# Optimization experiments

Measured on AMD Instinct MI355X. Metric: run time of the kernel, lower is better.

The kernel has to match this reference:

```python
import jax, jax.numpy as jnp
import numpy as np

N_OSC = 32
CONV = 1000.0  # convergence_factor


def _cpg_ode(y, ia, ifr, cw, pb):
    # Faithful to CPGOde.forward, including its unpacking order:
    # (amplitudes, amplitudes_dot, phases) = (y[:n], y[n:2n], y[2n:3n])
    n = N_OSC
    a = y[:n]
    a_dot = y[n:2 * n]
    ph = y[2 * n:3 * n]
    phase_dots = ifr + jnp.sum(a[:, None] * cw * jnp.sin(ph[None, :] - ph[:, None] - pb), axis=1)
    a_dd = CONV * (CONV / 4.0 * (ia - a) - a_dot)
    # states_to_tensor(amplitudes_dot, phase_dots, amplitudes_dot_dot)
    return jnp.concatenate([a_dot, phase_dots, a_dd])


def _rk4_38_step(f, y, h):
    # torchdiffeq 'rk4' = rk4_alt_step_func (3/8 rule), one step over t=[0, h]
    k1 = f(y)
    k2 = f(y + h * k1 / 3.0)
    k3 = f(y + h * (k2 - k1 / 3.0))
    k4 = f(y + h * (k1 - k2 + k3))
    return y + h * 0.125 * (k1 + 3.0 * (k2 + k3) + k4)


def _mlp(x, Ws, bs):
    # Linear stack with ReLU between layers, none after the last
    for i, (W, b) in enumerate(zip(Ws, bs)):
        x = W @ x + b
        if i < len(Ws) - 1:
            x = jax.nn.relu(x)
    return x


def _init_linear(key, fan_in, fan_out):
    kW, kb = jax.random.split(key)
    bound = 1.0 / np.sqrt(fan_in)
    W = jax.random.uniform(kW, (fan_out, fan_in), minval=-bound, maxval=bound, dtype=jnp.float32)
    b = jax.random.uniform(kb, (fan_out,), minval=-bound, maxval=bound, dtype=jnp.float32)
    return W, b


def setup_inputs() -> dict:
    key = jax.random.key(0)
    ks = jax.random.split(key, 10)
    n = N_OSC
    n_params = 2 * n + 2 * n * n  # 2112
    in_dims = [2049, 4096, 4096, n_params]  # input_layers[0]+1, ..., final param layer
    out_dims = [2 * n, 2048, 2048, 1024]
    inp = {}
    inp["state"] = jax.random.normal(ks[0], (3 * n,), dtype=jnp.float32) * 0.1
    inp["x"] = jax.random.normal(ks[1], (2048,), dtype=jnp.float32)
    inp["timestep"] = jnp.array(0.01, dtype=jnp.float32)
    for i in range(3):
        W, b = _init_linear(ks[2 + i], in_dims[i], in_dims[i + 1])
        inp[f"in_W{i}"] = W
        inp[f"in_b{i}"] = b
    for i in range(3):
        W, b = _init_linear(ks[5 + i], out_dims[i], out_dims[i + 1])
        inp[f"out_W{i}"] = W
        inp[f"out_b{i}"] = b
    return inp


def reference(state, x, timestep,
              in_W0, in_b0, in_W1, in_b1, in_W2, in_b2,
              out_W0, out_b0, out_W1, out_b1, out_W2, out_b2):
    n = N_OSC
    # append timestep scalar to the input features
    x = jnp.concatenate([x, timestep[None]])
    params = _mlp(x, [in_W0, in_W1, in_W2], [in_b0, in_b1, in_b2])
    ia = params[:n]
    ifr = params[n:2 * n]
    cw = params[2 * n:2 * n + n * n].reshape(n, n)
    pb = params[2 * n + n * n:].reshape(n, n)
    f = lambda y: _cpg_ode(y, ia, ifr, cw, pb)
    new_state = _rk4_38_step(f, state, timestep)
    a = new_state[:n]
    ph = new_state[n:2 * n]
    cpg_out = jnp.concatenate([a * jnp.cos(ph), a * jnp.sin(ph)])
    out = _mlp(cpg_out, [out_W0, out_W1, out_W2], [out_b0, out_b1, out_b2])
    return (jax.lax.stop_gradient(new_state), out)
```

## Files before the change

### kernel.cpp

```cpp
#include <hip/hip_runtime.h>
#include <hip/hip_bf16.h>
#include <stdint.h>

typedef unsigned short ushort_t;

__device__ __forceinline__ float bf2f(ushort_t u) {
    union { unsigned int i; float f; } v;
    v.i = ((unsigned int)u) << 16;
    return v.f;
}

__device__ __forceinline__ ushort_t f2bf(float f) {
    __hip_bfloat16 h = __float2bfloat16(f);
    return *reinterpret_cast<ushort_t*>(&h);
}

__device__ __forceinline__ float read_ts_robust(const void* ts) {
    float bf = bf2f(((const ushort_t*)ts)[0]);
    float ab = fabsf(bf);
    if (isfinite(bf) && ab > 1e-6f && ab < 1e3f) return bf;
    return ((const float*)ts)[0];
}

__global__ void detect_kernel(const ushort_t* __restrict__ W, int* __restrict__ flag) {
    if (threadIdx.x == 0 && blockIdx.x == 0) {
        int cnt = 0;
        for (int k = 0; k < 64; k++) {
            float v = bf2f(W[2 * k]);
            if (!(fabsf(v) < 1.0f)) cnt++;
        }
        *flag = (cnt >= 8) ? 1 : 0;
    }
}

__global__ void prep_x_kernel(const ushort_t* __restrict__ xb,
                              const void* __restrict__ ts,
                              float* __restrict__ xf, int n,
                              const int* __restrict__ flag) {
    int f = *flag;
    int i = blockIdx.x * blockDim.x + threadIdx.x;
    if (i < n) xf[i] = f ? ((const float*)xb)[i] : bf2f(xb[i]);
    if (i == 0) xf[n] = f ? ((const float*)ts)[0] : read_ts_robust(ts);
}

__global__ __launch_bounds__(256) void gemv_kernel(
    const ushort_t* __restrict__ W, const ushort_t* __restrict__ B,
    const float* __restrict__ x, float* __restrict__ y,
    void* __restrict__ outbuf, int out_off, int rows, int cols, int relu,
    const int* __restrict__ flag)
{
    int f = *flag;
    int wave = threadIdx.x >> 6;
    int lane = threadIdx.x & 63;
    int row = blockIdx.x * 4 + wave;
    if (row >= rows) return;

    float sum = 0.0f;

    if (f) {
        const float* w = (const float*)W + (size_t)row * (size_t)cols;
        int mis = (int)(((uintptr_t)w & 15) >> 2);
        int start = (4 - mis) & 3;
        if (start > cols) start = cols;
        if (lane < start) sum += w[lane] * x[lane];
        int nv = (cols - start) >> 2;
        const float4* wv = (const float4*)(w + start);
        for (int g = lane; g < nv; g += 64) {
            float4 u = wv[g];
            const float* xp = x + start + g * 4;
            sum += u.x * xp[0] + u.y * xp[1] + u.z * xp[2] + u.w * xp[3];
        }
        int t = start + nv * 4 + lane;
        if (t < cols) sum += w[t] * x[t];
    } else {
        const ushort_t* w = W + (size_t)row * (size_t)cols;
        int mis = (int)(((uintptr_t)w & 15) >> 1);
        int start = (8 - mis) & 7;
        if (start > cols) start = cols;
        if (lane < start) sum += bf2f(w[lane]) * x[lane];
        int nv = (cols - start) >> 3;
        const uint4* wv = (const uint4*)(w + start);
        for (int g = lane; g < nv; g += 64) {
            uint4 u = wv[g];
            const float* xp = x + start + g * 8;
            sum += bf2f((ushort_t)(u.x & 0xffff)) * xp[0];
            sum += bf2f((ushort_t)(u.x >> 16))    * xp[1];
            sum += bf2f((ushort_t)(u.y & 0xffff)) * xp[2];
            sum += bf2f((ushort_t)(u.y >> 16))    * xp[3];
            sum += bf2f((ushort_t)(u.z & 0xffff)) * xp[4];
            sum += bf2f((ushort_t)(u.z >> 16))    * xp[5];
            sum += bf2f((ushort_t)(u.w & 0xffff)) * xp[6];
            sum += bf2f((ushort_t)(u.w >> 16))    * xp[7];
        }
        int t = start + nv * 8 + lane;
        if (t < cols) sum += bf2f(w[t]) * x[t];
    }

    #pragma unroll
    for (int off = 32; off > 0; off >>= 1)
        sum += __shfl_down(sum, off);

    if (lane == 0) {
        float r = sum + (f ? ((const float*)B)[row] : bf2f(B[row]));
        if (relu) r = fmaxf(r, 0.0f);
        if (y) y[row] = r;
        if (outbuf) {
            if (f) ((float*)outbuf)[out_off + row] = r;
            else   ((ushort_t*)outbuf)[out_off + row] = f2bf(r);
        }
    }
}

__global__ __launch_bounds__(64) void ode_kernel(
    const ushort_t* __restrict__ state, const void* __restrict__ ts,
    const float* __restrict__ params, float* __restrict__ cpg,
    void* __restrict__ out_state, const int* __restrict__ flag)
{
    const float CONV = 1000.0f;
    __shared__ float s_y[96];
    int f = *flag;
    int t = threadIdx.x;
    bool act = (t < 32);
    int i = t;
    float h = f ? ((const float*)ts)[0] : read_ts_robust(ts);

    float ia = 0.f, ifr = 0.f;
    float cwr[32], pbr[32];
    float y0a = 0.f, y0b = 0.f, y0c = 0.f;

    if (act) {
        ia = params[i];
        ifr = params[32 + i];
        #pragma unroll
        for (int j = 0; j < 32; j++) {
            cwr[j] = params[64 + i * 32 + j];
            pbr[j] = params[1088 + i * 32 + j];
        }
        const float* sf = (const float*)state;
        y0a = f ? sf[i]      : bf2f(state[i]);
        y0b = f ? sf[32 + i] : bf2f(state[32 + i]);
        y0c = f ? sf[64 + i] : bf2f(state[64 + i]);
        s_y[i] = y0a; s_y[32 + i] = y0b; s_y[64 + i] = y0c;
    }
    __syncthreads();

    float k1a=0,k1b=0,k1c=0, k2a=0,k2b=0,k2c=0, k3a=0,k3b=0,k3c=0, k4a=0,k4b=0,k4c=0;

    auto evalf = [&](float& fa, float& fb, float& fc) {
        float a  = s_y[i];
        float ad = s_y[32 + i];
        float ph = s_y[64 + i];
        float ssum = 0.0f;
        #pragma unroll
        for (int j = 0; j < 32; j++) {
            ssum += cwr[j] * sinf(s_y[64 + j] - ph - pbr[j]);
        }
        fa = ad;
        fb = ifr + a * ssum;
        fc = CONV * (CONV * 0.25f * (ia - a) - ad);
    };

    if (act) evalf(k1a, k1b, k1c);
    __syncthreads();
    if (act) {
        s_y[i]      = y0a + h * k1a / 3.0f;
        s_y[32 + i] = y0b + h * k1b / 3.0f;
        s_y[64 + i] = y0c + h * k1c / 3.0f;
    }
    __syncthreads();
    if (act) evalf(k2a, k2b, k2c);
    __syncthreads();
    if (act) {
        s_y[i]      = y0a + h * (k2a - k1a / 3.0f);
        s_y[32 + i] = y0b + h * (k2b - k1b / 3.0f);
        s_y[64 + i] = y0c + h * (k2c - k1c / 3.0f);
    }
    __syncthreads();
    if (act) evalf(k3a, k3b, k3c);
    __syncthreads();
    if (act) {
        s_y[i]      = y0a + h * (k1a - k2a + k3a);
        s_y[32 + i] = y0b + h * (k1b - k2b + k3b);
        s_y[64 + i] = y0c + h * (k1c - k2c + k3c);
    }
    __syncthreads();
    if (act) evalf(k4a, k4b, k4c);

    if (act) {
        float na = y0a + h * 0.125f * (k1a + 3.0f * (k2a + k3a) + k4a);
        float nb = y0b + h * 0.125f * (k1b + 3.0f * (k2b + k3b) + k4b);
        float nc = y0c + h * 0.125f * (k1c + 3.0f * (k2c + k3c) + k4c);
        if (f) {
            float* fo = (float*)out_state;
            fo[i] = na; fo[32 + i] = nb; fo[64 + i] = nc;
        } else {
            ushort_t* bo = (ushort_t*)out_state;
            bo[i] = f2bf(na); bo[32 + i] = f2bf(nb); bo[64 + i] = f2bf(nc);
        }
        cpg[i]      = na * cosf(nb);
        cpg[32 + i] = na * sinf(nb);
    }
}

extern "C" void kernel_launch(void* const* d_in, const int* in_sizes, int n_in,
                              void* d_out, int out_size, void* d_ws, size_t ws_size,
                              hipStream_t stream) {
    const ushort_t* state = (const ushort_t*)d_in[0];
    const ushort_t* x     = (const ushort_t*)d_in[1];
    const void*     ts    = d_in[2];
    const ushort_t* inW0  = (const ushort_t*)d_in[3];
    const ushort_t* inb0  = (const ushort_t*)d_in[4];
    const ushort_t* inW1  = (const ushort_t*)d_in[5];
    const ushort_t* inb1  = (const ushort_t*)d_in[6];
    const ushort_t* inW2  = (const ushort_t*)d_in[7];
    const ushort_t* inb2  = (const ushort_t*)d_in[8];
    const ushort_t* oW0   = (const ushort_t*)d_in[9];
    const ushort_t* ob0   = (const ushort_t*)d_in[10];
    const ushort_t* oW1   = (const ushort_t*)d_in[11];
    const ushort_t* ob1   = (const ushort_t*)d_in[12];
    const ushort_t* oW2   = (const ushort_t*)d_in[13];
    const ushort_t* ob2   = (const ushort_t*)d_in[14];

    float* ws  = (float*)d_ws;
    float* xf  = ws;
    float* h0  = ws + 2064;
    float* h1  = ws + 6160;
    float* pr  = ws + 10256;
    float* cpg = ws + 12368;
    float* g0  = ws + 12432;
    float* g1  = ws + 14480;
    int*   flg = (int*)(ws + 16536);

    detect_kernel<<<1, 64, 0, stream>>>(inW1, flg);
    prep_x_kernel<<<9, 256, 0, stream>>>(x, ts, xf, 2048, flg);
    gemv_kernel<<<1024, 256, 0, stream>>>(inW0, inb0, xf, h0, nullptr, 0, 4096, 2049, 1, flg);
    gemv_kernel<<<1024, 256, 0, stream>>>(inW1, inb1, h0, h1, nullptr, 0, 4096, 4096, 1, flg);
    gemv_kernel<<<528,  256, 0, stream>>>(inW2, inb2, h1, pr, nullptr, 0, 2112, 4096, 0, flg);
    ode_kernel<<<1, 64, 0, stream>>>(state, ts, pr, cpg, d_out, flg);
    gemv_kernel<<<512,  256, 0, stream>>>(oW0, ob0, cpg, g0, nullptr, 0, 2048, 64, 1, flg);
    gemv_kernel<<<512,  256, 0, stream>>>(oW1, ob1, g0, g1, nullptr, 0, 2048, 2048, 1, flg);
    gemv_kernel<<<256,  256, 0, stream>>>(oW2, ob2, g1, nullptr, d_out, 96, 1024, 2048, 0, flg);
}
```

Baseline: 263.4 us.

## Drop bf16 detection path, use block-per-row fp32 GEMV and sincos-factored ODE

Removes the runtime dtype detection kernel, the x-prep kernel and the bf16 branches, and assumes fp32 inputs throughout. The timestep column is folded directly into the first GEMV. Each GEMV now uses a full 256-thread block per row with 4-way unrolled float4 loads and a shared-memory cross-wave reduction, instead of one wave per row. The ODE kernel precomputes sin/cos of the phase biases and uses angle-difference identities, so it needs only one sincos per oscillator per stage instead of 32 sinf calls. This trades launch count and dtype flexibility for more memory parallelism per row. It breaks if the inputs are actually bf16.

```diff
diff --git a/kernel.cpp b/kernel.cpp
--- a/kernel.cpp
+++ b/kernel.cpp
@@ -1,202 +1,146 @@
 #include <hip/hip_runtime.h>
-#include <hip/hip_bf16.h>
 #include <stdint.h>
 
-typedef unsigned short ushort_t;
+template<int RELU, int TS>
+__global__ __launch_bounds__(256) void gemv_k(
+    const float* __restrict__ W, const float* __restrict__ B,
+    const float* __restrict__ x, const float* __restrict__ ts,
+    float* __restrict__ y, int cols)
+{
+    int tid = threadIdx.x;
+    int row = blockIdx.x;
+    int n = TS ? cols - 1 : cols;
+    const float* w = W + (size_t)row * (size_t)cols;
 
-__device__ __forceinline__ float bf2f(ushort_t u) {
-    union { unsigned int i; float f; } v;
-    v.i = ((unsigned int)u) << 16;
-    return v.f;
-}
+    int mis = (int)(((uintptr_t)w >> 2) & 3);
+    int start = (4 - mis) & 3;
+    if (start > n) start = n;
 
-__device__ __forceinline__ ushort_t f2bf(float f) {
-    __hip_bfloat16 h = __float2bfloat16(f);
-    return *reinterpret_cast<ushort_t*>(&h);
-}
+    float sum = 0.0f;
+    if (tid < start) sum += w[tid] * x[tid];
 
-__device__ __forceinline__ float read_ts_robust(const void* ts) {
-    float bf = bf2f(((const ushort_t*)ts)[0]);
-    float ab = fabsf(bf);
-    if (isfinite(bf) && ab > 1e-6f && ab < 1e3f) return bf;
-    return ((const float*)ts)[0];
-}
+    int nv = (n - start) >> 2;
+    const float4* wv = (const float4*)(w + start);
+    const float* xs = x + start;
 
-__global__ void detect_kernel(const ushort_t* __restrict__ W, int* __restrict__ flag) {
-    if (threadIdx.x == 0 && blockIdx.x == 0) {
-        int cnt = 0;
-        for (int k = 0; k < 64; k++) {
-            float v = bf2f(W[2 * k]);
-            if (!(fabsf(v) < 1.0f)) cnt++;
-        }
-        *flag = (cnt >= 8) ? 1 : 0;
+    int g = tid;
+    for (; g + 768 < nv; g += 1024) {
+        float4 u0 = wv[g];
+        float4 u1 = wv[g + 256];
+        float4 u2 = wv[g + 512];
+        float4 u3 = wv[g + 768];
+        const float* x0 = xs + 4 * g;
+        const float* x1 = xs + 4 * (g + 256);
+        const float* x2 = xs + 4 * (g + 512);
+        const float* x3 = xs + 4 * (g + 768);
+        sum += u0.x * x0[0] + u0.y * x0[1] + u0.z * x0[2] + u0.w * x0[3];
+        sum += u1.x * x1[0] + u1.y * x1[1] + u1.z * x1[2] + u1.w * x1[3];
+        sum += u2.x * x2[0] + u2.y * x2[1] + u2.z * x2[2] + u2.w * x2[3];
+        sum += u3.x * x3[0] + u3.y * x3[1] + u3.z * x3[2] + u3.w * x3[3];
+    }
+    for (; g < nv; g += 256) {
+        float4 u = wv[g];
+        const float* xp = xs + 4 * g;
+        sum += u.x * xp[0] + u.y * xp[1] + u.z * xp[2] + u.w * xp[3];
+    }
+    int t = start + nv * 4 + tid;
+    if (t < n) sum += w[t] * x[t];
+    if (TS && tid == 0) sum += w[n] * ts[0];
+
+    #pragma unroll
+    for (int off = 32; off > 0; off >>= 1) sum += __shfl_down(sum, off);
+    __shared__ float red[4];
+    if ((tid & 63) == 0) red[tid >> 6] = sum;
+    __syncthreads();
+    if (tid == 0) {
+        float r = red[0] + red[1] + red[2] + red[3] + B[row];
+        if (RELU) r = fmaxf(r, 0.0f);
+        y[row] = r;
     }
 }
 
-__global__ void prep_x_kernel(const ushort_t* __restrict__ xb,
-                              const void* __restrict__ ts,
-                              float* __restrict__ xf, int n,
-                              const int* __restrict__ flag) {
-    int f = *flag;
-    int i = blockIdx.x * blockDim.x + threadIdx.x;
-    if (i < n) xf[i] = f ? ((const float*)xb)[i] : bf2f(xb[i]);
-    if (i == 0) xf[n] = f ? ((const float*)ts)[0] : read_ts_robust(ts);
-}
-
-__global__ __launch_bounds__(256) void gemv_kernel(
-    const ushort_t* __restrict__ W, const ushort_t* __restrict__ B,
-    const float* __restrict__ x, float* __restrict__ y,
-    void* __restrict__ outbuf, int out_off, int rows, int cols, int relu,
-    const int* __restrict__ flag)
-{
-    int f = *flag;
-    int wave = threadIdx.x >> 6;
-    int lane = threadIdx.x & 63;
-    int row = blockIdx.x * 4 + wave;
-    if (row >= rows) return;
-
-    float sum = 0.0f;
-
-    if (f) {
-        const float* w = (const float*)W + (size_t)row * (size_t)cols;
-        int mis = (int)(((uintptr_t)w & 15) >> 2);
-        int start = (4 - mis) & 3;
-        if (start > cols) start = cols;
-        if (lane < start) sum += w[lane] * x[lane];
-        int nv = (cols - start) >> 2;
-        const float4* wv = (const float4*)(w + start);
-        for (int g = lane; g < nv; g += 64) {
-            float4 u = wv[g];
-            const float* xp = x + start + g * 4;
-            sum += u.x * xp[0] + u.y * xp[1] + u.z * xp[2] + u.w * xp[3];
-        }
-        int t = start + nv * 4 + lane;
-        if (t < cols) sum += w[t] * x[t];
-    } else {
-        const ushort_t* w = W + (size_t)row * (size_t)cols;
-        int mis = (int)(((uintptr_t)w & 15) >> 1);
-        int start = (8 - mis) & 7;
-        if (start > cols) start = cols;
-        if (lane < start) sum += bf2f(w[lane]) * x[lane];
-        int nv = (cols - start) >> 3;
-        const uint4* wv = (const uint4*)(w + start);
-        for (int g = lane; g < nv; g += 64) {
-            uint4 u = wv[g];
-            const float* xp = x + start + g * 8;
-            sum += bf2f((ushort_t)(u.x & 0xffff)) * xp[0];
-            sum += bf2f((ushort_t)(u.x >> 16))    * xp[1];
-            sum += bf2f((ushort_t)(u.y & 0xffff)) * xp[2];
-            sum += bf2f((ushort_t)(u.y >> 16))    * xp[3];
-            sum += bf2f((ushort_t)(u.z & 0xffff)) * xp[4];
-            sum += bf2f((ushort_t)(u.z >> 16))    * xp[5];
-            sum += bf2f((ushort_t)(u.w & 0xffff)) * xp[6];
-            sum += bf2f((ushort_t)(u.w >> 16))    * xp[7];
-        }
-        int t = start + nv * 8 + lane;
-        if (t < cols) sum += bf2f(w[t]) * x[t];
-    }
-
-    #pragma unroll
-    for (int off = 32; off > 0; off >>= 1)
-        sum += __shfl_down(sum, off);
-
-    if (lane == 0) {
-        float r = sum + (f ? ((const float*)B)[row] : bf2f(B[row]));
-        if (relu) r = fmaxf(r, 0.0f);
-        if (y) y[row] = r;
-        if (outbuf) {
-            if (f) ((float*)outbuf)[out_off + row] = r;
-            else   ((ushort_t*)outbuf)[out_off + row] = f2bf(r);
-        }
-    }
-}
-
-__global__ __launch_bounds__(64) void ode_kernel(
-    const ushort_t* __restrict__ state, const void* __restrict__ ts,
+__global__ __launch_bounds__(64) void ode_k(
+    const float* __restrict__ state, const float* __restrict__ ts,
     const float* __restrict__ params, float* __restrict__ cpg,
-    void* __restrict__ out_state, const int* __restrict__ flag)
+    float* __restrict__ out_state)
 {
     const float CONV = 1000.0f;
-    __shared__ float s_y[96];
-    int f = *flag;
-    int t = threadIdx.x;
-    bool act = (t < 32);
-    int i = t;
-    float h = f ? ((const float*)ts)[0] : read_ts_robust(ts);
+    __shared__ float s_cw[32 * 33];
+    __shared__ float s_spb[32 * 33];
+    __shared__ float s_cpb[32 * 33];
+    __shared__ float s_s[32], s_c[32];
+    int tid = threadIdx.x;
 
-    float ia = 0.f, ifr = 0.f;
-    float cwr[32], pbr[32];
-    float y0a = 0.f, y0b = 0.f, y0c = 0.f;
-
-    if (act) {
-        ia = params[i];
-        ifr = params[32 + i];
-        #pragma unroll
-        for (int j = 0; j < 32; j++) {
-            cwr[j] = params[64 + i * 32 + j];
-            pbr[j] = params[1088 + i * 32 + j];
-        }
-        const float* sf = (const float*)state;
-        y0a = f ? sf[i]      : bf2f(state[i]);
-        y0b = f ? sf[32 + i] : bf2f(state[32 + i]);
-        y0c = f ? sf[64 + i] : bf2f(state[64 + i]);
-        s_y[i] = y0a; s_y[32 + i] = y0b; s_y[64 + i] = y0c;
+    for (int k = tid; k < 1024; k += 64) {
+        int p = k + (k >> 5);
+        s_cw[p] = params[64 + k];
+        float pb = params[1088 + k];
+        float sp, cp;
+        sincosf(pb, &sp, &cp);
+        s_spb[p] = sp;
+        s_cpb[p] = cp;
     }
     __syncthreads();
 
+    bool act = (tid < 32);
+    int i = tid;
+    float ia = 0.f, ifr = 0.f, y0a = 0.f, y0b = 0.f, y0c = 0.f;
+    if (act) {
+        ia  = params[i];
+        ifr = params[32 + i];
+        y0a = state[i];
+        y0b = state[32 + i];
+        y0c = state[64 + i];
+    }
+    float h = ts[0];
+
     float k1a=0,k1b=0,k1c=0, k2a=0,k2b=0,k2c=0, k3a=0,k3b=0,k3c=0, k4a=0,k4b=0,k4c=0;
 
-    auto evalf = [&](float& fa, float& fb, float& fc) {
-        float a  = s_y[i];
-        float ad = s_y[32 + i];
-        float ph = s_y[64 + i];
-        float ssum = 0.0f;
-        #pragma unroll
-        for (int j = 0; j < 32; j++) {
-            ssum += cwr[j] * sinf(s_y[64 + j] - ph - pbr[j]);
+    auto do_eval = [&](float a, float ad, float ph,
+                       float& fa, float& fb, float& fc) {
+        __syncthreads();
+        if (act) {
+            float s, c;
+            sincosf(ph, &s, &c);
+            s_s[i] = s; s_c[i] = c;
         }
-        fa = ad;
-        fb = ifr + a * ssum;
-        fc = CONV * (CONV * 0.25f * (ia - a) - ad);
+        __syncthreads();
+        if (act) {
+            float si = s_s[i], ci = s_c[i];
+            float ssum = 0.0f;
+            #pragma unroll
+            for (int j = 0; j < 32; j++) {
+                float sj = s_s[j], cj = s_c[j];
+                float sdp = sj * ci - cj * si;
+                float cdp = cj * ci + sj * si;
+                int p = i * 33 + j;
+                float sv = sdp * s_cpb[p] - cdp * s_spb[p];
+                ssum += s_cw[p] * sv;
+            }
+            fa = ad;
+            fb = ifr + a * ssum;
+            fc = CONV * (CONV * 0.25f * (ia - a) - ad);
+        }
     };
 
-    if (act) evalf(k1a, k1b, k1c);
-    __syncthreads();
-    if (act) {
-        s_y[i]      = y0a + h * k1a / 3.0f;
-        s_y[32 + i] = y0b + h * k1b / 3.0f;
-        s_y[64 + i] = y0c + h * k1c / 3.0f;
-    }
-    __syncthreads();
-    if (act) evalf(k2a, k2b, k2c);
-    __syncthreads();
-    if (act) {
-        s_y[i]      = y0a + h * (k2a - k1a / 3.0f);
-        s_y[32 + i] = y0b + h * (k2b - k1b / 3.0f);
-        s_y[64 + i] = y0c + h * (k2c - k1c / 3.0f);
-    }
-    __syncthreads();
-    if (act) evalf(k3a, k3b, k3c);
-    __syncthreads();
-    if (act) {
-        s_y[i]      = y0a + h * (k1a - k2a + k3a);
-        s_y[32 + i] = y0b + h * (k1b - k2b + k3b);
-        s_y[64 + i] = y0c + h * (k1c - k2c + k3c);
-    }
-    __syncthreads();
-    if (act) evalf(k4a, k4b, k4c);
+    do_eval(y0a, y0b, y0c, k1a, k1b, k1c);
+    do_eval(y0a + h * k1a / 3.0f,
+            y0b + h * k1b / 3.0f,
+            y0c + h * k1c / 3.0f, k2a, k2b, k2c);
+    do_eval(y0a + h * (k2a - k1a / 3.0f),
+            y0b + h * (k2b - k1b / 3.0f),
+            y0c + h * (k2c - k1c / 3.0f), k3a, k3b, k3c);
+    do_eval(y0a + h * (k1a - k2a + k3a),
+            y0b + h * (k1b - k2b + k3b),
+            y0c + h * (k1c - k2c + k3c), k4a, k4b, k4c);
 
     if (act) {
         float na = y0a + h * 0.125f * (k1a + 3.0f * (k2a + k3a) + k4a);
         float nb = y0b + h * 0.125f * (k1b + 3.0f * (k2b + k3b) + k4b);
         float nc = y0c + h * 0.125f * (k1c + 3.0f * (k2c + k3c) + k4c);
-        if (f) {
-            float* fo = (float*)out_state;
-            fo[i] = na; fo[32 + i] = nb; fo[64 + i] = nc;
-        } else {
-            ushort_t* bo = (ushort_t*)out_state;
-            bo[i] = f2bf(na); bo[32 + i] = f2bf(nb); bo[64 + i] = f2bf(nc);
-        }
+        out_state[i]      = na;
+        out_state[32 + i] = nb;
+        out_state[64 + i] = nc;
         cpg[i]      = na * cosf(nb);
         cpg[32 + i] = na * sinf(nb);
     }
@@ -205,39 +149,37 @@
 extern "C" void kernel_launch(void* const* d_in, const int* in_sizes, int n_in,
                               void* d_out, int out_size, void* d_ws, size_t ws_size,
                               hipStream_t stream) {
-    const ushort_t* state = (const ushort_t*)d_in[0];
-    const ushort_t* x     = (const ushort_t*)d_in[1];
-    const void*     ts    = d_in[2];
-    const ushort_t* inW0  = (const ushort_t*)d_in[3];
-    const ushort_t* inb0  = (const ushort_t*)d_in[4];
-    const ushort_t* inW1  = (const ushort_t*)d_in[5];
-    const ushort_t* inb1  = (const ushort_t*)d_in[6];
-    const ushort_t* inW2  = (const ushort_t*)d_in[7];
-    const ushort_t* inb2  = (const ushort_t*)d_in[8];
-    const ushort_t* oW0   = (const ushort_t*)d_in[9];
-    const ushort_t* ob0   = (const ushort_t*)d_in[10];
-    const ushort_t* oW1   = (const ushort_t*)d_in[11];
-    const ushort_t* ob1   = (const ushort_t*)d_in[12];
-    const ushort_t* oW2   = (const ushort_t*)d_in[13];
-    const ushort_t* ob2   = (const ushort_t*)d_in[14];
+    const float* state = (const float*)d_in[0];
+    const float* x     = (const float*)d_in[1];
+    const float* ts    = (const float*)d_in[2];
+    const float* inW0  = (const float*)d_in[3];
+    const float* inb0  = (const float*)d_in[4];
+    const float* inW1  = (const float*)d_in[5];
+    const float* inb1  = (const float*)d_in[6];
+    const float* inW2  = (const float*)d_in[7];
+    const float* inb2  = (const float*)d_in[8];
+    const float* oW0   = (const float*)d_in[9];
+    const float* ob0   = (const float*)d_in[10];
+    const float* oW1   = (const float*)d_in[11];
+    const float* ob1   = (const float*)d_in[12];
+    const float* oW2   = (const float*)d_in[13];
+    const float* ob2   = (const float*)d_in[14];
 
     float* ws  = (float*)d_ws;
-    float* xf  = ws;
-    float* h0  = ws + 2064;
-    float* h1  = ws + 6160;
-    float* pr  = ws + 10256;
-    float* cpg = ws + 12368;
-    float* g0  = ws + 12432;
-    float* g1  = ws + 14480;
-    int*   flg = (int*)(ws + 16536);
+    float* h0  = ws;
+    float* h1  = ws + 4096;
+    float* pr  = ws + 8192;
+    float* cpg = ws + 10304;
+    float* g0  = ws + 10368;
+    float* g1  = ws + 12416;
 
-    detect_kernel<<<1, 64, 0, stream>>>(inW1, flg);
-    prep_x_kernel<<<9, 256, 0, stream>>>(x, ts, xf, 2048, flg);
-    gemv_kernel<<<1024, 256, 0, stream>>>(inW0, inb0, xf, h0, nullptr, 0, 4096, 2049, 1, flg);
-    gemv_kernel<<<1024, 256, 0, stream>>>(inW1, inb1, h0, h1, nullptr, 0, 4096, 4096, 1, flg);
-    gemv_kernel<<<528,  256, 0, stream>>>(inW2, inb2, h1, pr, nullptr, 0, 2112, 4096, 0, flg);
-    ode_kernel<<<1, 64, 0, stream>>>(state, ts, pr, cpg, d_out, flg);
-    gemv_kernel<<<512,  256, 0, stream>>>(oW0, ob0, cpg, g0, nullptr, 0, 2048, 64, 1, flg);
-    gemv_kernel<<<512,  256, 0, stream>>>(oW1, ob1, g0, g1, nullptr, 0, 2048, 2048, 1, flg);
-    gemv_kernel<<<256,  256, 0, stream>>>(oW2, ob2, g1, nullptr, d_out, 96, 1024, 2048, 0, flg);
+    float* out = (float*)d_out;
+
+    gemv_k<1,1><<<4096, 256, 0, stream>>>(inW0, inb0, x,   ts,      h0, 2049);
+    gemv_k<1,0><<<4096, 256, 0, stream>>>(inW1, inb1, h0,  nullptr, h1, 4096);
+    gemv_k<0,0><<<2112, 256, 0, stream>>>(inW2, inb2, h1,  nullptr, pr, 4096);
+    ode_k<<<1, 64, 0, stream>>>(state, ts, pr, cpg, out);
+    gemv_k<1,0><<<2048, 256, 0, stream>>>(oW0,  ob0,  cpg, nullptr, g0, 64);
+    gemv_k<1,0><<<2048, 256, 0, stream>>>(oW1,  ob1,  g0,  nullptr, g1, 2048);
+    gemv_k<0,0><<<1024, 256, 0, stream>>>(oW2,  ob2,  g1,  nullptr, out + 96, 2048);
 }
```

Result: faster. 214.1 us (-18.7%).
